# Kernel tuning notes

Measured on AMD Instinct MI355X. Metric: run time of the kernel, lower is better.

Reference implementation:

```python
import jax, jax.numpy as jnp
import numpy as np

N_HARMONIC = 6
CONCAT = (3,)  # cfg.append_distance: concat embedding after this layer index
N_LAYERS = 8


def harmonic_embedding(x):
    # x: [N, 3] -> [N, 6*2*3 + 3] = [N, 39]
    freqs = 2.0 ** jnp.arange(N_HARMONIC, dtype=x.dtype)  # omega0 = 1.0, logspace
    embed = (x[..., None] * freqs).reshape(*x.shape[:-1], -1)  # [N, 18]
    return jnp.concatenate([jnp.sin(embed), jnp.cos(embed), x], axis=-1)


def setup_inputs() -> dict:
    key = jax.random.key(0)
    N, H, E = 262144, 256, 39
    ks = jax.random.split(key, 11)
    inp = {"points": jax.random.normal(ks[0], (N, 3), dtype=jnp.float32)}
    in_dims = [E, H, H, H, E + H, H, H, H]  # skip-concat before layer 4
    for i, d_in in enumerate(in_dims):
        scale = 1.0 / np.sqrt(d_in)
        inp[f"w{i}"] = jax.random.normal(ks[i + 1], (d_in, H), dtype=jnp.float32) * scale
        inp[f"b{i}"] = jnp.zeros((H,), dtype=jnp.float32)
    inp["wsdf"] = jax.random.normal(ks[9], (H, 1), dtype=jnp.float32) * (1.0 / np.sqrt(H))
    inp["bsdf"] = jnp.zeros((1,), dtype=jnp.float32)
    return inp


def reference(points, w0, b0, w1, b1, w2, b2, w3, b3, w4, b4, w5, b5, w6, b6, w7, b7, wsdf, bsdf):
    ws = [w0, w1, w2, w3, w4, w5, w6, w7]
    bs = [b0, b1, b2, b3, b4, b5, b6, b7]
    emb = harmonic_embedding(points.reshape(-1, 3))  # [N, 39]
    x = emb
    for i in range(N_LAYERS):
        x = jax.nn.relu(x @ ws[i] + bs[i])
        if i in CONCAT:
            x = jnp.concatenate([emb, x], axis=-1)  # torch.cat([add, xyz])
    return x @ wsdf + bsdf  # [N, 1] signed distance
```

## Files before the change

### kernel.cpp

```cpp
#include <hip/hip_runtime.h>
#include <hip/hip_fp16.h>

typedef _Float16 f16x8 __attribute__((ext_vector_type(8)));
typedef _Float16 f16x4 __attribute__((ext_vector_type(4)));
typedef float    f32x16 __attribute__((ext_vector_type(16)));
typedef float    f32x4 __attribute__((ext_vector_type(4)));

#define SH 264
#define SE 56

struct LayerPtrs {
  const float* w[8];
  const float* b[8];
};

__global__ void prep_weights(LayerPtrs P, f16x8* __restrict__ wf) {
  int gid = blockIdx.x * 256 + threadIdx.x;
  if (gid >= 60416) return;
  const int OFF[9] = {0,1536,9728,17920,26112,35840,44032,52224,60416};
  int l = 0;
  while (gid >= OFF[l+1]) ++l;
  int f = gid - OFF[l];
  int lane = f & 63;
  int t = f >> 6;
  int mtile = t & 7;
  int kc = t >> 3;
  int col = mtile * 32 + (lane & 31);
  int kb  = (lane >> 5) * 8;
  const float* w = P.w[l];
  f16x8 v;
#pragma unroll
  for (int j = 0; j < 8; ++j) {
    float x = 0.f;
    if (l == 4) {
      if (kc < 3) {
        int k = kc * 16 + kb + j;
        if (k < 39) x = w[k * 256 + col];
      } else {
        int k = (kc - 3) * 16 + kb + j;
        x = w[(39 + k) * 256 + col];
      }
    } else if (l == 0) {
      int k = kc * 16 + kb + j;
      if (k < 39) x = w[k * 256 + col];
    } else {
      int k = kc * 16 + kb + j;
      x = w[k * 256 + col];
    }
    v[j] = (_Float16)x;
  }
  wf[gid] = v;
}

template<int NKC>
__device__ __forceinline__ void mm(const f16x8* __restrict__ wb,
                                   const _Float16* __restrict__ b0,
                                   const _Float16* __restrict__ b1,
                                   f32x16 acc[2][2]) {
#pragma unroll
  for (int kc = 0; kc < NKC; ++kc) {
    f16x8 a0 = wb[(kc * 8 + 0) * 64];
    f16x8 a1 = wb[(kc * 8 + 1) * 64];
    f16x8 v0 = *(const f16x8*)(b0 + kc * 16);
    f16x8 v1 = *(const f16x8*)(b1 + kc * 16);
    acc[0][0] = __builtin_amdgcn_mfma_f32_32x32x16_f16(a0, v0, acc[0][0], 0, 0, 0);
    acc[0][1] = __builtin_amdgcn_mfma_f32_32x32x16_f16(a0, v1, acc[0][1], 0, 0, 0);
    acc[1][0] = __builtin_amdgcn_mfma_f32_32x32x16_f16(a1, v0, acc[1][0], 0, 0, 0);
    acc[1][1] = __builtin_amdgcn_mfma_f32_32x32x16_f16(a1, v1, acc[1][1], 0, 0, 0);
  }
}

__device__ __forceinline__ void zero_acc(f32x16 acc[2][2]) {
#pragma unroll
  for (int mt = 0; mt < 2; ++mt)
#pragma unroll
    for (int nt = 0; nt < 2; ++nt)
#pragma unroll
      for (int r = 0; r < 16; ++r) acc[mt][nt][r] = 0.f;
}

__device__ __forceinline__ void store_act(f32x16 acc[2][2], const float* __restrict__ bp,
                                          int wv, int lane, _Float16* __restrict__ H) {
  int p0 = lane & 31, h = lane >> 5;
#pragma unroll
  for (int mt = 0; mt < 2; ++mt) {
    int hb = wv * 64 + mt * 32 + 4 * h;
#pragma unroll
    for (int g = 0; g < 4; ++g) {
      f32x4 bv = *(const f32x4*)&bp[hb + 8 * g];
#pragma unroll
      for (int nt = 0; nt < 2; ++nt) {
        f16x4 o;
#pragma unroll
        for (int r = 0; r < 4; ++r) {
          float x = acc[mt][nt][4 * g + r] + bv[r];
          o[r] = (_Float16)fmaxf(x, 0.f);
        }
        *(f16x4*)&H[(nt * 32 + p0) * SH + hb + 8 * g] = o;
      }
    }
  }
}

__global__ __launch_bounds__(256, 4)
void mlp_fused(const float* __restrict__ points,
               LayerPtrs P,
               const f16x8* __restrict__ wf,
               const float* __restrict__ wsdf,
               const float* __restrict__ bsdf,
               float* __restrict__ out) {
  __shared__ __align__(16) _Float16 H[64 * SH];
  __shared__ __align__(16) _Float16 E[64 * SE];
  const int tid = threadIdx.x;
  const int blk = blockIdx.x;

  if (tid < 64) {
    int p = blk * 64 + tid;
    float xyz[3] = {points[p * 3 + 0], points[p * 3 + 1], points[p * 3 + 2]};
    _Float16* row = &E[tid * SE];
#pragma unroll
    for (int c = 0; c < 3; ++c) {
      float fr = 1.f;
#pragma unroll
      for (int k = 0; k < 6; ++k) {
        float e = xyz[c] * fr;
        row[c * 6 + k]      = (_Float16)sinf(e);
        row[18 + c * 6 + k] = (_Float16)cosf(e);
        fr *= 2.f;
      }
      row[36 + c] = (_Float16)xyz[c];
    }
    for (int c = 39; c < SE; ++c) row[c] = (_Float16)0.f;
  }
  __syncthreads();

  const int lane = tid & 63;
  const int wv   = tid >> 6;
  const int p0   = lane & 31;
  const int h    = lane >> 5;

  const _Float16* e0 = &E[p0 * SE + h * 8];
  const _Float16* e1 = &E[(32 + p0) * SE + h * 8];
  const _Float16* h0 = &H[p0 * SH + h * 8];
  const _Float16* h1 = &H[(32 + p0) * SH + h * 8];
  const f16x8* wb = wf + wv * 128 + lane;

  const int WOFF[8] = {0,1536,9728,17920,26112,35840,44032,52224};

  f32x16 acc[2][2];

  zero_acc(acc);
  mm<3>(wb + WOFF[0], e0, e1, acc);
  store_act(acc, P.b[0], wv, lane, H);
  __syncthreads();

#pragma unroll
  for (int l = 1; l < 4; ++l) {
    zero_acc(acc);
    mm<16>(wb + WOFF[l], h0, h1, acc);
    __syncthreads();
    store_act(acc, P.b[l], wv, lane, H);
    __syncthreads();
  }

  zero_acc(acc);
  mm<3>(wb + WOFF[4], e0, e1, acc);
  mm<16>(wb + WOFF[4] + 3 * 512, h0, h1, acc);
  __syncthreads();
  store_act(acc, P.b[4], wv, lane, H);
  __syncthreads();

#pragma unroll
  for (int l = 5; l < 8; ++l) {
    zero_acc(acc);
    mm<16>(wb + WOFF[l], h0, h1, acc);
    __syncthreads();
    store_act(acc, P.b[l], wv, lane, H);
    __syncthreads();
  }

  {
    const int p = tid >> 2, part = tid & 3;
    float a = 0.f;
    const _Float16* xr = &H[p * SH + part * 64];
#pragma unroll
    for (int j = 0; j < 8; ++j) {
      f16x8 hh = *(const f16x8*)&xr[j * 8];
      f32x4 wa = *(const f32x4*)&wsdf[part * 64 + j * 8];
      f32x4 wc = *(const f32x4*)&wsdf[part * 64 + j * 8 + 4];
      a += (float)hh[0] * wa[0] + (float)hh[1] * wa[1]
         + (float)hh[2] * wa[2] + (float)hh[3] * wa[3]
         + (float)hh[4] * wc[0] + (float)hh[5] * wc[1]
         + (float)hh[6] * wc[2] + (float)hh[7] * wc[3];
    }
    a += __shfl_down(a, 1);
    a += __shfl_down(a, 2);
    if (part == 0) out[blk * 64 + p] = a + bsdf[0];
  }
}

extern "C" void kernel_launch(void* const* d_in, const int* in_sizes, int n_in,
                              void* d_out, int out_size, void* d_ws, size_t ws_size,
                              hipStream_t stream) {
  const float* points = (const float*)d_in[0];
  LayerPtrs P;
  for (int i = 0; i < 8; ++i) {
    P.w[i] = (const float*)d_in[1 + 2 * i];
    P.b[i] = (const float*)d_in[2 + 2 * i];
  }
  const float* wsdf = (const float*)d_in[17];
  const float* bsdf = (const float*)d_in[18];
  f16x8* wf = (f16x8*)d_ws;

  int N = in_sizes[0] / 3;
  prep_weights<<<236, 256, 0, stream>>>(P, wf);
  mlp_fused<<<N / 64, 256, 0, stream>>>(points, P, wf, wsdf, bsdf, (float*)d_out);
}
```

Baseline: 354.3 us.

## Process 128 points per block to reuse weight fragments across four MFMA column tiles

Doubles the number of points per workgroup from 64 to 128, so each wave computes 2x4 MFMA tiles and each weight fragment loaded from global memory feeds twice as many MFMAs. The point is to halve weight traffic per point and amortise the block barriers. In exchange it doubles accumulator registers and LDS per block, so occupancy is lowered to 2 blocks per SIMD group. The embedding stride also shrinks to 48, and the final reduction is reworked to use 2 threads per point.

```diff
diff --git a/kernel.cpp b/kernel.cpp
--- a/kernel.cpp
+++ b/kernel.cpp
@@ -7,7 +7,8 @@
 typedef float    f32x4 __attribute__((ext_vector_type(4)));
 
 #define SH 264
-#define SE 56
+#define SE 48
+#define PTS 128
 
 struct LayerPtrs {
   const float* w[8];
@@ -52,34 +53,42 @@
   wf[gid] = v;
 }
 
-template<int NKC>
+template<int NKC, int STRIDE>
 __device__ __forceinline__ void mm(const f16x8* __restrict__ wb,
                                    const _Float16* __restrict__ b0,
                                    const _Float16* __restrict__ b1,
-                                   f32x16 acc[2][2]) {
+                                   const _Float16* __restrict__ b2,
+                                   const _Float16* __restrict__ b3,
+                                   f32x16 acc[2][4]) {
 #pragma unroll
   for (int kc = 0; kc < NKC; ++kc) {
     f16x8 a0 = wb[(kc * 8 + 0) * 64];
     f16x8 a1 = wb[(kc * 8 + 1) * 64];
     f16x8 v0 = *(const f16x8*)(b0 + kc * 16);
     f16x8 v1 = *(const f16x8*)(b1 + kc * 16);
+    f16x8 v2 = *(const f16x8*)(b2 + kc * 16);
+    f16x8 v3 = *(const f16x8*)(b3 + kc * 16);
     acc[0][0] = __builtin_amdgcn_mfma_f32_32x32x16_f16(a0, v0, acc[0][0], 0, 0, 0);
     acc[0][1] = __builtin_amdgcn_mfma_f32_32x32x16_f16(a0, v1, acc[0][1], 0, 0, 0);
+    acc[0][2] = __builtin_amdgcn_mfma_f32_32x32x16_f16(a0, v2, acc[0][2], 0, 0, 0);
+    acc[0][3] = __builtin_amdgcn_mfma_f32_32x32x16_f16(a0, v3, acc[0][3], 0, 0, 0);
     acc[1][0] = __builtin_amdgcn_mfma_f32_32x32x16_f16(a1, v0, acc[1][0], 0, 0, 0);
     acc[1][1] = __builtin_amdgcn_mfma_f32_32x32x16_f16(a1, v1, acc[1][1], 0, 0, 0);
-  }
-}
-
-__device__ __forceinline__ void zero_acc(f32x16 acc[2][2]) {
+    acc[1][2] = __builtin_amdgcn_mfma_f32_32x32x16_f16(a1, v2, acc[1][2], 0, 0, 0);
+    acc[1][3] = __builtin_amdgcn_mfma_f32_32x32x16_f16(a1, v3, acc[1][3], 0, 0, 0);
+  }
+}
+
+__device__ __forceinline__ void zero_acc(f32x16 acc[2][4]) {
 #pragma unroll
   for (int mt = 0; mt < 2; ++mt)
 #pragma unroll
-    for (int nt = 0; nt < 2; ++nt)
+    for (int nt = 0; nt < 4; ++nt)
 #pragma unroll
       for (int r = 0; r < 16; ++r) acc[mt][nt][r] = 0.f;
 }
 
-__device__ __forceinline__ void store_act(f32x16 acc[2][2], const float* __restrict__ bp,
+__device__ __forceinline__ void store_act(f32x16 acc[2][4], const float* __restrict__ bp,
                                           int wv, int lane, _Float16* __restrict__ H) {
   int p0 = lane & 31, h = lane >> 5;
 #pragma unroll
@@ -89,7 +98,7 @@
     for (int g = 0; g < 4; ++g) {
       f32x4 bv = *(const f32x4*)&bp[hb + 8 * g];
 #pragma unroll
-      for (int nt = 0; nt < 2; ++nt) {
+      for (int nt = 0; nt < 4; ++nt) {
         f16x4 o;
 #pragma unroll
         for (int r = 0; r < 4; ++r) {
@@ -102,20 +111,20 @@
   }
 }
 
-__global__ __launch_bounds__(256, 4)
+__global__ __launch_bounds__(256, 2)
 void mlp_fused(const float* __restrict__ points,
                LayerPtrs P,
                const f16x8* __restrict__ wf,
                const float* __restrict__ wsdf,
                const float* __restrict__ bsdf,
                float* __restrict__ out) {
-  __shared__ __align__(16) _Float16 H[64 * SH];
-  __shared__ __align__(16) _Float16 E[64 * SE];
+  __shared__ __align__(16) _Float16 H[PTS * SH];
+  __shared__ __align__(16) _Float16 E[PTS * SE];
   const int tid = threadIdx.x;
   const int blk = blockIdx.x;
 
-  if (tid < 64) {
-    int p = blk * 64 + tid;
+  if (tid < PTS) {
+    int p = blk * PTS + tid;
     float xyz[3] = {points[p * 3 + 0], points[p * 3 + 1], points[p * 3 + 2]};
     _Float16* row = &E[tid * SE];
 #pragma unroll
@@ -130,6 +139,7 @@
       }
       row[36 + c] = (_Float16)xyz[c];
     }
+#pragma unroll
     for (int c = 39; c < SE; ++c) row[c] = (_Float16)0.f;
   }
   __syncthreads();
@@ -141,31 +151,35 @@
 
   const _Float16* e0 = &E[p0 * SE + h * 8];
   const _Float16* e1 = &E[(32 + p0) * SE + h * 8];
+  const _Float16* e2 = &E[(64 + p0) * SE + h * 8];
+  const _Float16* e3 = &E[(96 + p0) * SE + h * 8];
   const _Float16* h0 = &H[p0 * SH + h * 8];
   const _Float16* h1 = &H[(32 + p0) * SH + h * 8];
+  const _Float16* h2 = &H[(64 + p0) * SH + h * 8];
+  const _Float16* h3 = &H[(96 + p0) * SH + h * 8];
   const f16x8* wb = wf + wv * 128 + lane;
 
   const int WOFF[8] = {0,1536,9728,17920,26112,35840,44032,52224};
 
-  f32x16 acc[2][2];
+  f32x16 acc[2][4];
 
   zero_acc(acc);
-  mm<3>(wb + WOFF[0], e0, e1, acc);
+  mm<3, SE>(wb + WOFF[0], e0, e1, e2, e3, acc);
   store_act(acc, P.b[0], wv, lane, H);
   __syncthreads();
 
 #pragma unroll
   for (int l = 1; l < 4; ++l) {
     zero_acc(acc);
-    mm<16>(wb + WOFF[l], h0, h1, acc);
+    mm<16, SH>(wb + WOFF[l], h0, h1, h2, h3, acc);
     __syncthreads();
     store_act(acc, P.b[l], wv, lane, H);
     __syncthreads();
   }
 
   zero_acc(acc);
-  mm<3>(wb + WOFF[4], e0, e1, acc);
-  mm<16>(wb + WOFF[4] + 3 * 512, h0, h1, acc);
+  mm<3, SE>(wb + WOFF[4], e0, e1, e2, e3, acc);
+  mm<16, SH>(wb + WOFF[4] + 3 * 512, h0, h1, h2, h3, acc);
   __syncthreads();
   store_act(acc, P.b[4], wv, lane, H);
   __syncthreads();
@@ -173,29 +187,28 @@
 #pragma unroll
   for (int l = 5; l < 8; ++l) {
     zero_acc(acc);
-    mm<16>(wb + WOFF[l], h0, h1, acc);
+    mm<16, SH>(wb + WOFF[l], h0, h1, h2, h3, acc);
     __syncthreads();
     store_act(acc, P.b[l], wv, lane, H);
     __syncthreads();
   }
 
   {
-    const int p = tid >> 2, part = tid & 3;
+    const int p = tid >> 1, part = tid & 1;
     float a = 0.f;
-    const _Float16* xr = &H[p * SH + part * 64];
-#pragma unroll
-    for (int j = 0; j < 8; ++j) {
+    const _Float16* xr = &H[p * SH + part * 128];
+#pragma unroll
+    for (int j = 0; j < 16; ++j) {
       f16x8 hh = *(const f16x8*)&xr[j * 8];
-      f32x4 wa = *(const f32x4*)&wsdf[part * 64 + j * 8];
-      f32x4 wc = *(const f32x4*)&wsdf[part * 64 + j * 8 + 4];
+      f32x4 wa = *(const f32x4*)&wsdf[part * 128 + j * 8];
+      f32x4 wc = *(const f32x4*)&wsdf[part * 128 + j * 8 + 4];
       a += (float)hh[0] * wa[0] + (float)hh[1] * wa[1]
          + (float)hh[2] * wa[2] + (float)hh[3] * wa[3]
          + (float)hh[4] * wc[0] + (float)hh[5] * wc[1]
          + (float)hh[6] * wc[2] + (float)hh[7] * wc[3];
     }
     a += __shfl_down(a, 1);
-    a += __shfl_down(a, 2);
-    if (part == 0) out[blk * 64 + p] = a + bsdf[0];
+    if (part == 0) out[blk * PTS + p] = a + bsdf[0];
   }
 }
 
@@ -214,5 +227,5 @@
 
   int N = in_sizes[0] / 3;
   prep_weights<<<236, 256, 0, stream>>>(P, wf);
-  mlp_fused<<<N / 64, 256, 0, stream>>>(points, P, wf, wsdf, bsdf, (float*)d_out);
-}
+  mlp_fused<<<N / PTS, 256, 0, stream>>>(points, P, wf, wsdf, bsdf, (float*)d_out);
+}
```

New measurement: 318.0 us. 10.3% less time.
